# Performance work log

Measured on AMD Instinct MI355X. Metric: run time of the kernel, lower is better.

Reference implementation:

```python
import jax, jax.numpy as jnp
import numpy as np

B, S, H = 1, 2048, 2048
NH = 16
Q_LORA, KV_LORA = 1536, 512
D_NOPE, D_ROPE, D_V = 128, 64, 128
D_QK = D_NOPE + D_ROPE  # 192
EPS = 1e-6
ROPE_BASE = 10000.0


def setup_inputs() -> dict:
    key = jax.random.key(0)
    ks = jax.random.split(key, 8)
    def lin(k, fan_in, fan_out):
        # nn.Linear default init, stored as [in, out] for x @ W
        bound = 1.0 / np.sqrt(fan_in)
        return jax.random.uniform(k, (fan_in, fan_out), jnp.float32, -bound, bound)
    return {
        "hidden_states": jax.random.normal(ks[0], (B, S, H), jnp.float32),
        "Wqa": lin(ks[1], H, Q_LORA),
        "q_a_ln_w": jnp.ones((Q_LORA,), jnp.float32),
        "Wqb": lin(ks[2], Q_LORA, NH * D_QK),
        "Wkva": lin(ks[3], H, KV_LORA + D_ROPE),
        "kv_a_ln_w": jnp.ones((KV_LORA,), jnp.float32),
        "Wkvb": lin(ks[4], KV_LORA, NH * (D_NOPE + D_V)),
        "Wo": lin(ks[5], NH * D_V, H),
    }


def _rmsnorm(x, w):
    xf = x.astype(jnp.float32)
    var = jnp.mean(xf * xf, axis=-1, keepdims=True)
    return w * (xf * jax.lax.rsqrt(var + EPS)).astype(x.dtype)


def _rotate_half(x):
    x1, x2 = jnp.split(x, 2, axis=-1)
    return jnp.concatenate((-x2, x1), axis=-1)


def _rope_tables(seq_len, dtype=jnp.float32):
    inv_freq = 1.0 / (ROPE_BASE ** (jnp.arange(0, D_ROPE, 2, dtype=jnp.float32) / D_ROPE))
    t = jnp.arange(seq_len, dtype=jnp.float32)
    freqs = jnp.outer(t, inv_freq)                      # [S, D_ROPE/2]
    emb = jnp.concatenate((freqs, freqs), axis=-1)      # [S, D_ROPE]
    return jnp.cos(emb).astype(dtype), jnp.sin(emb).astype(dtype)


def reference(hidden_states, Wqa, q_a_ln_w, Wqb, Wkva, kv_a_ln_w, Wkvb, Wo):
    bsz, q_len, _ = hidden_states.shape
    scale = D_QK ** -0.5

    # Q path: LoRA down -> RMSNorm -> up
    q = _rmsnorm(hidden_states @ Wqa, q_a_ln_w) @ Wqb            # [B,S,NH*D_QK]
    q = q.reshape(bsz, q_len, NH, D_QK).transpose(0, 2, 1, 3)    # [B,NH,S,D_QK]
    q_nope, q_pe = q[..., :D_NOPE], q[..., D_NOPE:]

    # KV path: compressed latent + shared rope key
    ckv = hidden_states @ Wkva                                    # [B,S,KV_LORA+D_ROPE]
    compressed_kv, k_pe = ckv[..., :KV_LORA], ckv[..., KV_LORA:]
    k_pe = k_pe.reshape(bsz, q_len, 1, D_ROPE).transpose(0, 2, 1, 3)  # [B,1,S,D_ROPE]
    kv = _rmsnorm(compressed_kv, kv_a_ln_w) @ Wkvb                # [B,S,NH*(D_NOPE+D_V)]
    kv = kv.reshape(bsz, q_len, NH, D_NOPE + D_V).transpose(0, 2, 1, 3)
    k_nope, v = kv[..., :D_NOPE], kv[..., D_NOPE:]                # [B,NH,S,D_NOPE], [B,NH,S,D_V]

    # decoupled RoPE on the rope sub-dims
    cos, sin = _rope_tables(q_len, hidden_states.dtype)
    cos = cos[None, None]  # [1,1,S,D_ROPE] broadcast over batch & heads
    sin = sin[None, None]
    q_pe = q_pe * cos + _rotate_half(q_pe) * sin
    k_pe = k_pe * cos + _rotate_half(k_pe) * sin                  # [B,1,S,D_ROPE]

    query = jnp.concatenate([q_nope, q_pe], axis=-1)              # [B,NH,S,D_QK]
    key = jnp.concatenate([k_nope, jnp.broadcast_to(k_pe, (bsz, NH, q_len, D_ROPE))], axis=-1)

    attn = jnp.einsum('bhqd,bhkd->bhqk', query, key) * scale      # [B,NH,S,S]
    causal = jnp.triu(jnp.ones((q_len, q_len), bool), k=1)
    attn = jnp.where(causal, -jnp.inf, attn)
    attn = jax.nn.softmax(attn.astype(jnp.float32), axis=-1).astype(query.dtype)

    out = jnp.einsum('bhqk,bhkd->bhqd', attn, v)                  # [B,NH,S,D_V]
    out = out.transpose(0, 2, 1, 3).reshape(bsz, q_len, NH * D_V)
    return out @ Wo                                               # [B,S,H]
```

## Files before the change

### kernel.cpp

```cpp
#include <hip/hip_runtime.h>
#include <hip/hip_bf16.h>
#include <math.h>

#define S_LEN 2048
#define H_DIM 2048
#define NH 16
#define Q_LORA 1536
#define KV_LORA 512
#define D_NOPE 128
#define D_ROPE 64
#define D_V 128
#define D_QK 192

typedef unsigned short ushort_t;
typedef __attribute__((ext_vector_type(8))) short short8;
typedef __attribute__((ext_vector_type(4))) float f32x4;

__device__ __forceinline__ ushort_t f2bf(float f) {
    unsigned int u = __float_as_uint(f);
    u = (u + 0x7FFFu + ((u >> 16) & 1u)) >> 16;
    return (ushort_t)u;
}
__device__ __forceinline__ float bf2f(ushort_t u) {
    return __uint_as_float(((unsigned int)u) << 16);
}

__device__ __forceinline__ void storeC(float* p, float v) { *p = v; }
__device__ __forceinline__ void storeC(ushort_t* p, float v) { *p = f2bf(v); }

__device__ __forceinline__ void gload_lds16(const ushort_t* g, ushort_t* l) {
    __builtin_amdgcn_global_load_lds(
        (const __attribute__((address_space(1))) unsigned int*)(const void*)g,
        (__attribute__((address_space(3))) unsigned int*)(void*)l, 16, 0, 0);
}

__device__ __forceinline__ float dpp_max16(float x) {
    x = fmaxf(x, __int_as_float(__builtin_amdgcn_update_dpp(0, __float_as_int(x), 0xB1, 0xF, 0xF, true)));
    x = fmaxf(x, __int_as_float(__builtin_amdgcn_update_dpp(0, __float_as_int(x), 0x4E, 0xF, 0xF, true)));
    x = fmaxf(x, __int_as_float(__builtin_amdgcn_update_dpp(0, __float_as_int(x), 0x124, 0xF, 0xF, true)));
    x = fmaxf(x, __int_as_float(__builtin_amdgcn_update_dpp(0, __float_as_int(x), 0x128, 0xF, 0xF, true)));
    return x;
}
__device__ __forceinline__ float dpp_sum16(float x) {
    x += __int_as_float(__builtin_amdgcn_update_dpp(0, __float_as_int(x), 0xB1, 0xF, 0xF, true));
    x += __int_as_float(__builtin_amdgcn_update_dpp(0, __float_as_int(x), 0x4E, 0xF, 0xF, true));
    x += __int_as_float(__builtin_amdgcn_update_dpp(0, __float_as_int(x), 0x124, 0xF, 0xF, true));
    x += __int_as_float(__builtin_amdgcn_update_dpp(0, __float_as_int(x), 0x128, 0xF, 0xF, true));
    return x;
}

__device__ __forceinline__ void convT_body(
    const float* __restrict__ W, ushort_t* __restrict__ Wt,
    int K, int N, int n0, int k0, float (*tile)[33])
{
    const int tr = threadIdx.x >> 5, tc = threadIdx.x & 31;
    #pragma unroll
    for (int i = 0; i < 4; ++i) {
        int r = tr + i * 8;
        float v = 0.f;
        if (n0 + tc < N) v = W[(size_t)(k0 + r) * N + n0 + tc];
        tile[r][tc] = v;
    }
    __syncthreads();
    #pragma unroll
    for (int i = 0; i < 4; ++i) {
        int r = tr + i * 8;
        Wt[(size_t)(n0 + r) * K + k0 + tc] = f2bf(tile[tc][r]);
    }
}

__global__ __launch_bounds__(256) void unified_conv(
    const float* __restrict__ hs, ushort_t* __restrict__ hs16,
    const float* __restrict__ Wqa, const float* __restrict__ Wkva,
    const float* __restrict__ Wqb, const float* __restrict__ Wkvb,
    const float* __restrict__ Wo,
    ushort_t* __restrict__ WcatT, ushort_t* __restrict__ WqbT,
    ushort_t* __restrict__ WkvbT, ushort_t* __restrict__ WoT)
{
    __shared__ float tile[32][33];
    int b = blockIdx.x;
    if (b < 4096) {
        int base = (b * 256 + threadIdx.x) * 4;
        float4 v = *(const float4*)(hs + base);
        hs16[base + 0] = f2bf(v.x);
        hs16[base + 1] = f2bf(v.y);
        hs16[base + 2] = f2bf(v.z);
        hs16[base + 3] = f2bf(v.w);
        return;
    }
    b -= 4096;
    const float* W; ushort_t* Wt; int K, N, nbx;
    if (b < 3072)        {            W = Wqa;  Wt = WcatT;                              K = 2048; N = 1536; nbx = 48;  }
    else if (b < 4352)   { b -= 3072; W = Wkva; Wt = WcatT + (size_t)Q_LORA * H_DIM;     K = 2048; N = 576;  nbx = 20;  }
    else if (b < 8960)   { b -= 4352; W = Wqb;  Wt = WqbT;                               K = 1536; N = 3072; nbx = 96;  }
    else if (b < 11008)  { b -= 8960; W = Wkvb; Wt = WkvbT;                              K = 512;  N = 4096; nbx = 128; }
    else                 { b -= 11008; W = Wo;  Wt = WoT;                                K = 2048; N = 2048; nbx = 64;  }
    convT_body(W, Wt, K, N, (b % nbx) * 32, (b / nbx) * 32, tile);
}

__global__ __launch_bounds__(256) void fused_norm_ropek(
    const ushort_t* __restrict__ cat16r, ushort_t* __restrict__ qa16,
    ushort_t* __restrict__ ckv16n, ushort_t* __restrict__ kpe16,
    const float* __restrict__ qlnw, const float* __restrict__ klnw)
{
    __shared__ float red[4];
    const int b = blockIdx.x;
    if (b < 4096) {
        const bool isQ = (b < 2048);
        const int row = isQ ? b : b - 2048;
        const int K = isQ ? Q_LORA : KV_LORA;
        const ushort_t* x = cat16r + (size_t)row * 2176 + (isQ ? 0 : Q_LORA);
        ushort_t* y = (isQ ? qa16 + (size_t)row * Q_LORA : ckv16n + (size_t)row * KV_LORA);
        const float* wv = isQ ? qlnw : klnw;
        float ss = 0.f;
        for (int i = threadIdx.x; i < K; i += 256) { float v = bf2f(x[i]); ss += v * v; }
        #pragma unroll
        for (int off = 32; off > 0; off >>= 1) ss += __shfl_down(ss, off);
        int lane = threadIdx.x & 63, wid = threadIdx.x >> 6;
        if (lane == 0) red[wid] = ss;
        __syncthreads();
        float tot = red[0] + red[1] + red[2] + red[3];
        float rs = rsqrtf(tot / (float)K + 1e-6f);
        for (int i = threadIdx.x; i < K; i += 256)
            y[i] = f2bf(bf2f(x[i]) * rs * wv[i]);
    } else {
        int idx = (b - 4096) * 256 + threadIdx.x;
        if (idx >= S_LEN * 32) return;
        int i = idx & 31;
        int s = idx >> 5;
        float inv = powf(10000.0f, -(2.0f * i) / 64.0f);
        float ang = (float)s * inv;
        float c = cosf(ang), sn = sinf(ang);
        const ushort_t* p = cat16r + (size_t)s * 2176 + Q_LORA + KV_LORA;
        ushort_t* q = kpe16 + (size_t)s * D_ROPE;
        float x1 = bf2f(p[i]), x2 = bf2f(p[i + 32]);
        q[i]      = f2bf(x1 * c - x2 * sn);
        q[i + 32] = f2bf(x2 * c + x1 * sn);
    }
}

__global__ __launch_bounds__(256) void conv_vT_kernel(
    const ushort_t* __restrict__ kv, ushort_t* __restrict__ v16t)
{
    __shared__ ushort_t tile[32][33];
    const int h = blockIdx.z;
    const int s0 = blockIdx.x * 32, d0 = blockIdx.y * 32;
    const int tr = threadIdx.x >> 5, tc = threadIdx.x & 31;
    #pragma unroll
    for (int i = 0; i < 4; ++i) {
        int r = tr + i * 8;
        tile[r][tc] = kv[(size_t)(s0 + r) * 4096 + h * 256 + D_NOPE + d0 + tc];
    }
    __syncthreads();
    #pragma unroll
    for (int i = 0; i < 4; ++i) {
        int r = tr + i * 8;
        v16t[(size_t)h * D_V * S_LEN + (size_t)(d0 + r) * S_LEN + s0 + tc] = tile[tc][r];
    }
}

template <typename CT>
__device__ __forceinline__ void gemm_body_bk64(
    const ushort_t* __restrict__ A, const ushort_t* __restrict__ Bt,
    CT* __restrict__ C, int N, int K, int m0, int n0,
    ushort_t* Al, ushort_t* Bl)
{
    const int tid = threadIdx.x;
    const int lane = tid & 63;
    const int w = tid >> 6;
    const int lm = lane & 15, quad = lane >> 4;
    const int wr = w >> 1, wc = w & 1;

    f32x4 acc[2][4];
    #pragma unroll
    for (int a = 0; a < 2; ++a)
        #pragma unroll
        for (int b = 0; b < 4; ++b) acc[a][b] = (f32x4){0.f, 0.f, 0.f, 0.f};

    const int rrow = tid >> 2;
    const int rcol = (tid & 3) * 8;

    for (int k0 = 0; k0 < K; k0 += 64) {
        __syncthreads();
        #pragma unroll
        for (int c = 0; c < 2; ++c) {
            gload_lds16(A + (size_t)(m0 + rrow) * K + k0 + c * 32 + rcol,
                        Al + c * 2048 + tid * 8);
            #pragma unroll
            for (int i = 0; i < 2; ++i)
                gload_lds16(Bt + (size_t)(n0 + i * 64 + rrow) * K + k0 + c * 32 + rcol,
                            Bl + c * 4096 + (i * 256 + tid) * 8);
        }
        __syncthreads();

        #pragma unroll
        for (int c = 0; c < 2; ++c) {
            short8 af[2], bf[4];
            #pragma unroll
            for (int t = 0; t < 2; ++t)
                af[t] = *(const short8*)(Al + c * 2048 + (wr * 32 + t * 16 + lm) * 32 + quad * 8);
            #pragma unroll
            for (int t = 0; t < 4; ++t)
                bf[t] = *(const short8*)(Bl + c * 4096 + (wc * 64 + t * 16 + lm) * 32 + quad * 8);
            #pragma unroll
            for (int mt = 0; mt < 2; ++mt)
                #pragma unroll
                for (int nt = 0; nt < 4; ++nt)
                    acc[mt][nt] = __builtin_amdgcn_mfma_f32_16x16x32_bf16(
                        af[mt], bf[nt], acc[mt][nt], 0, 0, 0);
        }
    }

    #pragma unroll
    for (int mt = 0; mt < 2; ++mt)
        #pragma unroll
        for (int nt = 0; nt < 4; ++nt)
            #pragma unroll
            for (int r = 0; r < 4; ++r) {
                int row = m0 + wr * 32 + mt * 16 + quad * 4 + r;
                int col = n0 + wc * 64 + nt * 16 + lm;
                storeC(&C[(size_t)row * N + col], acc[mt][nt][r]);
            }
}

template <typename CT>
__global__ __launch_bounds__(256) void mfma_gemm_bt(
    const ushort_t* __restrict__ A, const ushort_t* __restrict__ Bt,
    CT* __restrict__ C, int N, int K)
{
    __shared__ ushort_t Al[2 * 64 * 32];
    __shared__ ushort_t Bl[2 * 128 * 32];
    gemm_body_bk64<CT>(A, Bt, C, N, K, blockIdx.y * 64, blockIdx.x * 128, Al, Bl);
}

__global__ __launch_bounds__(256) void mfma_gemm_dual(
    const ushort_t* __restrict__ A1, const ushort_t* __restrict__ Bt1,
    ushort_t* __restrict__ C1, int N1, int K1, int nb1,
    const ushort_t* __restrict__ A2, const ushort_t* __restrict__ Bt2,
    ushort_t* __restrict__ C2, int N2, int K2)
{
    __shared__ ushort_t Al[2 * 64 * 32];
    __shared__ ushort_t Bl[2 * 128 * 32];
    int g = blockIdx.x;
    if (g < nb1) {
        int nbx = N1 / 128;
        gemm_body_bk64<ushort_t>(A1, Bt1, C1, N1, K1, (g / nbx) * 64, (g % nbx) * 128, Al, Bl);
    } else {
        g -= nb1;
        int nbx = N2 / 128;
        gemm_body_bk64<ushort_t>(A2, Bt2, C2, N2, K2, (g / nbx) * 64, (g % nbx) * 128, Al, Bl);
    }
}

__device__ __forceinline__ void softmax_step(
    f32x4 s[4], int k0, int qw, int lm, int quad,
    float m_[4], float l_[4], f32x4 O[8], ushort_t* ps)
{
    const float scale = 0.07216878364870322f;
    #pragma unroll
    for (int r = 0; r < 4; ++r) {
        int qrow = qw + quad * 4 + r;
        float a[4];
        #pragma unroll
        for (int st = 0; st < 4; ++st)
            a[st] = (k0 + st * 16 + lm <= qrow) ? s[st][r] * scale : -1e30f;
        float mx = dpp_max16(fmaxf(fmaxf(a[0], a[1]), fmaxf(a[2], a[3])));
        float mn = fmaxf(m_[r], mx);
        float p[4];
        #pragma unroll
        for (int st = 0; st < 4; ++st) p[st] = __expf(a[st] - mn);
        float alpha = __expf(m_[r] - mn);
        float psum = dpp_sum16((p[0] + p[1]) + (p[2] + p[3]));
        l_[r] = l_[r] * alpha + psum;
        m_[r] = mn;
        #pragma unroll
        for (int c = 0; c < 8; ++c) O[c][r] *= alpha;
        #pragma unroll
        for (int st = 0; st < 4; ++st)
            ps[(quad * 4 + r) * 72 + st * 16 + lm] = f2bf(p[st]);
    }
}

__global__ __launch_bounds__(128) void mla_attn_kernel(
    const ushort_t* __restrict__ qb, const ushort_t* __restrict__ kvb,
    const ushort_t* __restrict__ kpe, const ushort_t* __restrict__ v16t,
    ushort_t* __restrict__ aout16)
{
    __shared__ ushort_t Kn[4 * 64 * 32];
    __shared__ ushort_t Kr[2 * 64 * 32];
    __shared__ ushort_t Vt[2 * 128 * 32];
    __shared__ ushort_t Ps[2][16][72];

    const int h = blockIdx.x;
    const int q0 = 32 * (63 - blockIdx.y);
    const int w = threadIdx.x >> 6;
    const int lane = threadIdx.x & 63;
    const int lm = lane & 15, quad = lane >> 4;
    const int qw = q0 + 16 * w;
    ushort_t* myPs = &Ps[w][0][0];

    short8 qf[6];
    #pragma unroll
    for (int f = 0; f < 6; ++f)
        qf[f] = *(const short8*)(qb + (size_t)(qw + lm) * 3072 + h * 192 + f * 32 + quad * 8);
    {
        float srow = (float)(qw + lm);
        #pragma unroll
        for (int j = 0; j < 8; ++j) {
            int i = quad * 8 + j;
            float inv = powf(10000.0f, -(2.0f * i) / 64.0f);
            float ang = srow * inv;
            float c = cosf(ang), sn = sinf(ang);
            float x1 = bf2f((ushort_t)qf[4][j]);
            float x2 = bf2f((ushort_t)qf[5][j]);
            qf[4][j] = (short)f2bf(x1 * c - x2 * sn);
            qf[5][j] = (short)f2bf(x2 * c + x1 * sn);
        }
    }

    f32x4 O[8];
    #pragma unroll
    for (int c = 0; c < 8; ++c) O[c] = (f32x4){0.f, 0.f, 0.f, 0.f};
    float m_[4] = {-1e30f, -1e30f, -1e30f, -1e30f};
    float l_[4] = {0.f, 0.f, 0.f, 0.f};

    const int skey = lane >> 2;
    const int ssub = (lane & 3) * 8;

    const int kend = q0 + 32;
    for (int k0 = 0; k0 < kend; k0 += 64) {
        __syncthreads();
        {
            #pragma unroll
            for (int fi = 0; fi < 2; ++fi) {
                int f = 2 * w + fi;
                #pragma unroll
                for (int i = 0; i < 4; ++i)
                    gload_lds16(kvb + (size_t)(k0 + i * 16 + skey) * 4096 + h * 256 + f * 32 + ssub,
                                Kn + f * 2048 + i * 512 + lane * 8);
            }
            #pragma unroll
            for (int i = 0; i < 4; ++i)
                gload_lds16(kpe + (size_t)(k0 + i * 16 + skey) * 64 + w * 32 + ssub,
                            Kr + w * 2048 + i * 512 + lane * 8);
            #pragma unroll
            for (int j = 0; j < 8; ++j)
                gload_lds16(v16t + ((size_t)h * 128 + j * 16 + skey) * S_LEN + k0 + w * 32 + ssub,
                            Vt + w * 4096 + j * 512 + lane * 8);
        }
        __syncthreads();

        if (k0 < qw + 16) {
            f32x4 s[4];
            #pragma unroll
            for (int st = 0; st < 4; ++st) s[st] = (f32x4){0.f, 0.f, 0.f, 0.f};
            #pragma unroll
            for (int f = 0; f < 4; ++f)
                #pragma unroll
                for (int st = 0; st < 4; ++st) {
                    short8 kf = *(const short8*)(Kn + f * 2048 + (st * 16 + lm) * 32 + quad * 8);
                    s[st] = __builtin_amdgcn_mfma_f32_16x16x32_bf16(qf[f], kf, s[st], 0, 0, 0);
                }
            #pragma unroll
            for (int f2 = 0; f2 < 2; ++f2)
                #pragma unroll
                for (int st = 0; st < 4; ++st) {
                    short8 kf = *(const short8*)(Kr + f2 * 2048 + (st * 16 + lm) * 32 + quad * 8);
                    s[st] = __builtin_amdgcn_mfma_f32_16x16x32_bf16(qf[4 + f2], kf, s[st], 0, 0, 0);
                }

            softmax_step(s, k0, qw, lm, quad, m_, l_, O, myPs);

            asm volatile("s_waitcnt lgkmcnt(0)" ::: "memory");
            short8 pf0 = *(const short8*)(myPs + lm * 72 + quad * 8);
            short8 pf1 = *(const short8*)(myPs + lm * 72 + 32 + quad * 8);
            #pragma unroll
            for (int c = 0; c < 8; ++c) {
                short8 vf0 = *(const short8*)(Vt + (c * 16 + lm) * 32 + quad * 8);
                short8 vf1 = *(const short8*)(Vt + 4096 + (c * 16 + lm) * 32 + quad * 8);
                O[c] = __builtin_amdgcn_mfma_f32_16x16x32_bf16(pf0, vf0, O[c], 0, 0, 0);
                O[c] = __builtin_amdgcn_mfma_f32_16x16x32_bf16(pf1, vf1, O[c], 0, 0, 0);
            }
        }
    }
    #pragma unroll
    for (int c = 0; c < 8; ++c)
        #pragma unroll
        for (int r = 0; r < 4; ++r) {
            int qrow = qw + quad * 4 + r;
            aout16[(size_t)qrow * 2048 + h * D_V + c * 16 + lm] = f2bf(O[c][r] / l_[r]);
        }
}

extern "C" void kernel_launch(void* const* d_in, const int* in_sizes, int n_in,
                              void* d_out, int out_size, void* d_ws, size_t ws_size,
                              hipStream_t stream)
{
    (void)in_sizes; (void)n_in; (void)out_size; (void)ws_size;
    const float* hs   = (const float*)d_in[0];
    const float* Wqa  = (const float*)d_in[1];
    const float* qlnw = (const float*)d_in[2];
    const float* Wqb  = (const float*)d_in[3];
    const float* Wkva = (const float*)d_in[4];
    const float* klnw = (const float*)d_in[5];
    const float* Wkvb = (const float*)d_in[6];
    const float* Wo   = (const float*)d_in[7];
    float* out = (float*)d_out;

    ushort_t* p = (ushort_t*)d_ws;
    ushort_t* hs16   = p; p += (size_t)S_LEN * H_DIM;
    ushort_t* WcatT  = p; p += (size_t)2176 * H_DIM;
    ushort_t* WqbT   = p; p += (size_t)3072 * Q_LORA;
    ushort_t* WkvbT  = p; p += (size_t)4096 * KV_LORA;
    ushort_t* WoT    = p; p += (size_t)H_DIM * H_DIM;
    ushort_t* cat16r = p; p += (size_t)S_LEN * 2176;
    ushort_t* qa16   = p; p += (size_t)S_LEN * Q_LORA;
    ushort_t* qbuf16 = p; p += (size_t)S_LEN * 3072;
    ushort_t* ckv16n = p; p += (size_t)S_LEN * KV_LORA;
    ushort_t* kpe16  = p; p += (size_t)S_LEN * D_ROPE;
    ushort_t* kv16   = p; p += (size_t)S_LEN * 4096;
    ushort_t* v16t   = p; p += (size_t)NH * D_V * S_LEN;
    ushort_t* aout16 = p; p += (size_t)S_LEN * 2048;

    unified_conv<<<19200, 256, 0, stream>>>(
        hs, hs16, Wqa, Wkva, Wqb, Wkvb, Wo, WcatT, WqbT, WkvbT, WoT);
    mfma_gemm_bt<ushort_t><<<dim3(2176 / 128, S_LEN / 64), 256, 0, stream>>>(
        hs16, WcatT, cat16r, 2176, H_DIM);
    fused_norm_ropek<<<4096 + 256, 256, 0, stream>>>(cat16r, qa16, ckv16n, kpe16, qlnw, klnw);
    mfma_gemm_dual<<<768 + 1024, 256, 0, stream>>>(
        qa16, WqbT, qbuf16, 3072, Q_LORA, 768,
        ckv16n, WkvbT, kv16, 4096, KV_LORA);
    conv_vT_kernel<<<dim3(S_LEN / 32, D_V / 32, NH), 256, 0, stream>>>(kv16, v16t);
    mla_attn_kernel<<<dim3(NH, 64), 128, 0, stream>>>(qbuf16, kv16, kpe16, v16t, aout16);
    mfma_gemm_bt<float><<<dim3(H_DIM / 128, S_LEN / 64), 256, 0, stream>>>(
        aout16, WoT, out, H_DIM, H_DIM);
}
```

Measured before the change: 336.8 us.

## Load K and V fragments directly from global memory, dropping LDS staging

New measurement: 478.6 us. 1.42x slower.

```diff
diff --git a/kernel.cpp b/kernel.cpp
--- a/kernel.cpp
+++ b/kernel.cpp
@@ -286,9 +286,6 @@
     const ushort_t* __restrict__ kpe, const ushort_t* __restrict__ v16t,
     ushort_t* __restrict__ aout16)
 {
-    __shared__ ushort_t Kn[4 * 64 * 32];
-    __shared__ ushort_t Kr[2 * 64 * 32];
-    __shared__ ushort_t Vt[2 * 128 * 32];
     __shared__ ushort_t Ps[2][16][72];
 
     const int h = blockIdx.x;
@@ -324,63 +321,41 @@
     float m_[4] = {-1e30f, -1e30f, -1e30f, -1e30f};
     float l_[4] = {0.f, 0.f, 0.f, 0.f};
 
-    const int skey = lane >> 2;
-    const int ssub = (lane & 3) * 8;
-
-    const int kend = q0 + 32;
+    const ushort_t* kn_base = kvb + (size_t)h * 256;
+    const ushort_t* vt_base = v16t + (size_t)h * 128 * S_LEN;
+
+    const int kend = qw + 16;
     for (int k0 = 0; k0 < kend; k0 += 64) {
-        __syncthreads();
-        {
-            #pragma unroll
-            for (int fi = 0; fi < 2; ++fi) {
-                int f = 2 * w + fi;
-                #pragma unroll
-                for (int i = 0; i < 4; ++i)
-                    gload_lds16(kvb + (size_t)(k0 + i * 16 + skey) * 4096 + h * 256 + f * 32 + ssub,
-                                Kn + f * 2048 + i * 512 + lane * 8);
+        f32x4 s[4];
+        #pragma unroll
+        for (int st = 0; st < 4; ++st) s[st] = (f32x4){0.f, 0.f, 0.f, 0.f};
+        #pragma unroll
+        for (int st = 0; st < 4; ++st) {
+            const ushort_t* krow = kn_base + (size_t)(k0 + st * 16 + lm) * 4096 + quad * 8;
+            #pragma unroll
+            for (int f = 0; f < 4; ++f) {
+                short8 kf = *(const short8*)(krow + f * 32);
+                s[st] = __builtin_amdgcn_mfma_f32_16x16x32_bf16(qf[f], kf, s[st], 0, 0, 0);
             }
-            #pragma unroll
-            for (int i = 0; i < 4; ++i)
-                gload_lds16(kpe + (size_t)(k0 + i * 16 + skey) * 64 + w * 32 + ssub,
-                            Kr + w * 2048 + i * 512 + lane * 8);
-            #pragma unroll
-            for (int j = 0; j < 8; ++j)
-                gload_lds16(v16t + ((size_t)h * 128 + j * 16 + skey) * S_LEN + k0 + w * 32 + ssub,
-                            Vt + w * 4096 + j * 512 + lane * 8);
-        }
-        __syncthreads();
-
-        if (k0 < qw + 16) {
-            f32x4 s[4];
-            #pragma unroll
-            for (int st = 0; st < 4; ++st) s[st] = (f32x4){0.f, 0.f, 0.f, 0.f};
-            #pragma unroll
-            for (int f = 0; f < 4; ++f)
-                #pragma unroll
-                for (int st = 0; st < 4; ++st) {
-                    short8 kf = *(const short8*)(Kn + f * 2048 + (st * 16 + lm) * 32 + quad * 8);
-                    s[st] = __builtin_amdgcn_mfma_f32_16x16x32_bf16(qf[f], kf, s[st], 0, 0, 0);
-                }
-            #pragma unroll
-            for (int f2 = 0; f2 < 2; ++f2)
-                #pragma unroll
-                for (int st = 0; st < 4; ++st) {
-                    short8 kf = *(const short8*)(Kr + f2 * 2048 + (st * 16 + lm) * 32 + quad * 8);
-                    s[st] = __builtin_amdgcn_mfma_f32_16x16x32_bf16(qf[4 + f2], kf, s[st], 0, 0, 0);
-                }
-
-            softmax_step(s, k0, qw, lm, quad, m_, l_, O, myPs);
-
-            asm volatile("s_waitcnt lgkmcnt(0)" ::: "memory");
-            short8 pf0 = *(const short8*)(myPs + lm * 72 + quad * 8);
-            short8 pf1 = *(const short8*)(myPs + lm * 72 + 32 + quad * 8);
-            #pragma unroll
-            for (int c = 0; c < 8; ++c) {
-                short8 vf0 = *(const short8*)(Vt + (c * 16 + lm) * 32 + quad * 8);
-                short8 vf1 = *(const short8*)(Vt + 4096 + (c * 16 + lm) * 32 + quad * 8);
-                O[c] = __builtin_amdgcn_mfma_f32_16x16x32_bf16(pf0, vf0, O[c], 0, 0, 0);
-                O[c] = __builtin_amdgcn_mfma_f32_16x16x32_bf16(pf1, vf1, O[c], 0, 0, 0);
-            }
+            const ushort_t* krp = kpe + (size_t)(k0 + st * 16 + lm) * 64 + quad * 8;
+            short8 kr0 = *(const short8*)(krp);
+            short8 kr1 = *(const short8*)(krp + 32);
+            s[st] = __builtin_amdgcn_mfma_f32_16x16x32_bf16(qf[4], kr0, s[st], 0, 0, 0);
+            s[st] = __builtin_amdgcn_mfma_f32_16x16x32_bf16(qf[5], kr1, s[st], 0, 0, 0);
+        }
+
+        softmax_step(s, k0, qw, lm, quad, m_, l_, O, myPs);
+
+        asm volatile("s_waitcnt lgkmcnt(0)" ::: "memory");
+        short8 pf0 = *(const short8*)(myPs + lm * 72 + quad * 8);
+        short8 pf1 = *(const short8*)(myPs + lm * 72 + 32 + quad * 8);
+        #pragma unroll
+        for (int c = 0; c < 8; ++c) {
+            const ushort_t* vr = vt_base + (size_t)(c * 16 + lm) * S_LEN + k0 + quad * 8;
+            short8 vf0 = *(const short8*)(vr);
+            short8 vf1 = *(const short8*)(vr + 32);
+            O[c] = __builtin_amdgcn_mfma_f32_16x16x32_bf16(pf0, vf0, O[c], 0, 0, 0);
+            O[c] = __builtin_amdgcn_mfma_f32_16x16x32_bf16(pf1, vf1, O[c], 0, 0, 0);
         }
     }
     #pragma unroll
```
